# Kernel optimization log

Measured on AMD Instinct MI355X. Metric: run time of the kernel, lower is better.

## Reference

```python
import jax, jax.numpy as jnp
import numpy as np

D = 256   # input_dim (also per-head dim)
H = 8     # num_heads
B = 32
S = 1024


def setup_inputs() -> dict:
    key = jax.random.key(0)
    ks = jax.random.split(key, 9)
    scale = 1.0 / np.sqrt(D)
    x = jax.random.normal(ks[0], (B, S, D), dtype=jnp.float32)
    Wk = jax.random.normal(ks[1], (D, D * H), dtype=jnp.float32) * scale
    bk = jnp.zeros((D * H,), dtype=jnp.float32)
    Wv = jax.random.normal(ks[2], (D, D * H), dtype=jnp.float32) * scale
    bv = jnp.zeros((D * H,), dtype=jnp.float32)
    query = jax.random.normal(ks[3], (H, D), dtype=jnp.float32)
    Wo = jax.random.normal(ks[4], (D * H, D), dtype=jnp.float32) / np.sqrt(D * H)
    bo = jnp.zeros((D,), dtype=jnp.float32)
    return {"x": x, "Wk": Wk, "bk": bk, "Wv": Wv, "bv": bv,
            "query": query, "Wo": Wo, "bo": bo}


def reference(x, Wk, bk, Wv, bv, query, Wo, bo):
    b, s, _ = x.shape
    # keys/values: [B, S, H, D]
    keys = (x @ Wk + bk).reshape(b, s, H, D)
    values = (x @ Wv + bv).reshape(b, s, H, D)
    # per-head single-query scores over sequence: [B, S, H]
    scores = jnp.einsum("bshd,hd->bsh", keys, query)
    attn = jax.nn.softmax(scores, axis=1)
    # attention-pooled values per head: [B, H, D] -> concat [B, H*D]
    pooled = jnp.einsum("bsh,bshd->bhd", attn, values).reshape(b, H * D)
    return pooled @ Wo + bo
```

## Files before the change

### kernel.cpp

```cpp
#include <hip/hip_runtime.h>

#define D 256
#define H 8
#define B 32
#define S 1024
#define SCH 32
#define SCS 32
#define XPAD 4

#define OFF_QK   0
#define OFF_ML   2048
#define OFF_XWP  18432

__global__ void __launch_bounds__(256) k_prep(
        const float* __restrict__ Wk, const float* __restrict__ query,
        const float* __restrict__ bo, float* __restrict__ qk,
        float* __restrict__ out) {
    const int h  = blockIdx.x >> 5;
    const int kc = blockIdx.x & 31;
    const int t  = threadIdx.x;
    const int kl = t >> 5;
    const int dq = t & 31;
    const int k  = kc * 8 + kl;
    const int d0 = dq * 8;
    const float* wrow = Wk + (size_t)k * (D * H) + h * D + d0;
    const float* qrow = query + h * D + d0;
    const float4 w0 = *(const float4*)(wrow);
    const float4 w1 = *(const float4*)(wrow + 4);
    const float4 q0 = *(const float4*)(qrow);
    const float4 q1 = *(const float4*)(qrow + 4);
    float acc = w0.x * q0.x + w0.y * q0.y + w0.z * q0.z + w0.w * q0.w
              + w1.x * q1.x + w1.y * q1.y + w1.z * q1.z + w1.w * q1.w;
    #pragma unroll
    for (int msk = 1; msk < 32; msk <<= 1) acc += __shfl_xor(acc, msk);
    if (dq == 0) qk[h * D + k] = acc;
    if (h == 0) out[(size_t)kc * D + t] = bo[t];
}

__global__ void __launch_bounds__(256, 4) k_fused(
        const float* __restrict__ x, const float* __restrict__ qk,
        float* __restrict__ xwp, float2* __restrict__ mlbuf) {
    const int b  = blockIdx.x >> 5;
    const int c  = blockIdx.x & 31;
    const int s0 = c * SCS;
    const int t  = threadIdx.x;
    __shared__ float xL[SCS][D + XPAD];
    __shared__ float sc[SCS][H];
    {
        const int sl = t >> 3;
        const int dq = t & 7;
        const int d0 = dq * 32;
        const float* xrow = x + ((size_t)(b * S + s0 + sl)) * D + d0;
        float4 xr[8];
        #pragma unroll
        for (int j0 = 0; j0 < 8; j0++) {
            xr[j0] = *(const float4*)(xrow + j0 * 4);
            *(float4*)(&xL[sl][d0 + j0 * 4]) = xr[j0];
        }
        float accA[H];
        #pragma unroll
        for (int hh = 0; hh < H; hh++) {
            const float* qb = qk + hh * D + d0;
            float a = 0.f;
            #pragma unroll
            for (int j0 = 0; j0 < 8; j0++) {
                const float4 qv = *(const float4*)(qb + j0 * 4);
                a += xr[j0].x * qv.x + xr[j0].y * qv.y
                   + xr[j0].z * qv.z + xr[j0].w * qv.w;
            }
            accA[hh] = a;
        }
        #pragma unroll
        for (int hh = 0; hh < H; hh++) {
            accA[hh] += __shfl_xor(accA[hh], 1);
            accA[hh] += __shfl_xor(accA[hh], 2);
            accA[hh] += __shfl_xor(accA[hh], 4);
        }
        if (dq == 0) {
            #pragma unroll
            for (int hh = 0; hh < H; hh++) sc[sl][hh] = accA[hh];
        }
    }
    __syncthreads();

    {
        const int hh = t >> 5;
        const int u  = t & 31;
        const float v = sc[u][hh];
        float m = v;
        #pragma unroll
        for (int msk = 1; msk < 32; msk <<= 1) m = fmaxf(m, __shfl_xor(m, msk));
        const float e = __expf(v - m);
        float sum = e;
        #pragma unroll
        for (int msk = 1; msk < 32; msk <<= 1) sum += __shfl_xor(sum, msk);
        sc[u][hh] = e;
        if (u == 0) mlbuf[((size_t)(b * H + hh)) * SCH + c] = make_float2(m, sum);
    }
    __syncthreads();

    {
        float acc2[H] = {};
        #pragma unroll 8
        for (int s = 0; s < SCS; s++) {
            const float xv = xL[s][t];
            const float4 pa = *(const float4*)(&sc[s][0]);
            const float4 pb = *(const float4*)(&sc[s][4]);
            acc2[0] += pa.x * xv; acc2[1] += pa.y * xv;
            acc2[2] += pa.z * xv; acc2[3] += pa.w * xv;
            acc2[4] += pb.x * xv; acc2[5] += pb.y * xv;
            acc2[6] += pb.z * xv; acc2[7] += pb.w * xv;
        }
        #pragma unroll
        for (int hh = 0; hh < H; hh++)
            xwp[(((size_t)(b * H + hh)) * SCH + c) * D + t] = acc2[hh];
    }
}

__global__ void __launch_bounds__(256, 4) k_po(
        const float* __restrict__ xwp, const float2* __restrict__ mlbuf,
        const float* __restrict__ Wv, const float* __restrict__ bv,
        const float* __restrict__ Wo, float* __restrict__ out) {
    const int blk = blockIdx.x;
    const int dvq = blk & 3;
    const int bh  = blk >> 2;
    const int b = bh >> 3, h = bh & 7;
    const int t = threadIdx.x;
    __shared__ float scaleL[SCH];
    __shared__ float xwL[D];
    __shared__ float pp[256];
    __shared__ float pooledL[64];

    if (t < SCH) {
        const float2 ml = mlbuf[((size_t)(b * H + h)) * SCH + t];
        float M = ml.x;
        #pragma unroll
        for (int msk = 1; msk < 32; msk <<= 1) M = fmaxf(M, __shfl_xor(M, msk));
        const float p = __expf(ml.x - M);
        float L = ml.y * p;
        #pragma unroll
        for (int msk = 1; msk < 32; msk <<= 1) L += __shfl_xor(L, msk);
        scaleL[t] = p / L;
    }
    __syncthreads();
    {
        const float* xp = xwp + ((size_t)(b * H + h)) * SCH * D + t;
        float acc = 0.f;
        #pragma unroll 8
        for (int cc = 0; cc < SCH; cc++)
            acc += xp[(size_t)cc * D] * scaleL[cc];
        xwL[t] = acc;
    }
    __syncthreads();
    {
        const int kseg = t >> 6;
        const int dvl  = t & 63;
        const float* wp = Wv + (size_t)(kseg * 64) * (D * H) + h * D + dvq * 64 + dvl;
        float acc = 0.f;
        #pragma unroll 8
        for (int dd = 0; dd < 64; dd++)
            acc += xwL[kseg * 64 + dd] * wp[(size_t)dd * (D * H)];
        pp[t] = acc;
    }
    __syncthreads();
    if (t < 64)
        pooledL[t] = pp[t] + pp[t + 64] + pp[t + 128] + pp[t + 192]
                   + bv[h * D + dvq * 64 + t];
    __syncthreads();
    {
        const float* wo = Wo + (size_t)(h * D + dvq * 64) * D + t;
        float acc = 0.f;
        #pragma unroll 8
        for (int dv = 0; dv < 64; dv++)
            acc += pooledL[dv] * wo[(size_t)dv * D];
        atomicAdd(out + (size_t)b * D + t, acc);
    }
}

extern "C" void kernel_launch(void* const* d_in, const int* in_sizes, int n_in,
                              void* d_out, int out_size, void* d_ws, size_t ws_size,
                              hipStream_t stream) {
    const float* x     = (const float*)d_in[0];
    const float* Wk    = (const float*)d_in[1];
    const float* Wv    = (const float*)d_in[3];
    const float* bv    = (const float*)d_in[4];
    const float* query = (const float*)d_in[5];
    const float* Wo    = (const float*)d_in[6];
    const float* bo    = (const float*)d_in[7];
    float* out = (float*)d_out;
    float* ws  = (float*)d_ws;

    float*  qk    = ws + OFF_QK;
    float2* mlbuf = (float2*)(ws + OFF_ML);
    float*  xwp   = ws + OFF_XWP;

    k_prep<<<dim3(H * 32), dim3(256), 0, stream>>>(Wk, query, bo, qk, out);
    k_fused<<<dim3(B * SCH), dim3(256), 0, stream>>>(x, qk, xwp, mlbuf);
    k_po<<<dim3(B * H * 4), dim3(256), 0, stream>>>(xwp, mlbuf, Wv, bv, Wo, out);
}
```

Before: 129.6 us.

## Double sequence chunk per block, stage qk in LDS, keep x in registers

The fused score/pool kernel now runs 512-thread blocks over 64-position chunks, which halves the partial buffers that the reduction kernel reads. The qk vectors are staged in shared memory instead of being read from global per thread. The x tile is no longer copied into shared memory; each half of the block re-reads its 32 rows into registers for the weighted sum. The two halves' partials are combined through a shared-memory stage. Reading x twice from global and the higher register count may cost bandwidth and occupancy. A rotated load order is also added.

```diff
diff --git a/kernel.cpp b/kernel.cpp
--- a/kernel.cpp
+++ b/kernel.cpp
@@ -4,13 +4,12 @@
 #define H 8
 #define B 32
 #define S 1024
-#define SCH 32
-#define SCS 32
-#define XPAD 4
+#define SCH 16
+#define SCS 64
 
 #define OFF_QK   0
 #define OFF_ML   2048
-#define OFF_XWP  18432
+#define OFF_XWP  10240
 
 __global__ void __launch_bounds__(256) k_prep(
         const float* __restrict__ Wk, const float* __restrict__ query,
@@ -37,15 +36,18 @@
     if (h == 0) out[(size_t)kc * D + t] = bo[t];
 }
 
-__global__ void __launch_bounds__(256, 4) k_fused(
+__global__ void __launch_bounds__(512, 2) k_fused(
         const float* __restrict__ x, const float* __restrict__ qk,
         float* __restrict__ xwp, float2* __restrict__ mlbuf) {
-    const int b  = blockIdx.x >> 5;
-    const int c  = blockIdx.x & 31;
+    const int b  = blockIdx.x >> 4;
+    const int c  = blockIdx.x & 15;
     const int s0 = c * SCS;
     const int t  = threadIdx.x;
-    __shared__ float xL[SCS][D + XPAD];
+    __shared__ float qkL[H * D];
     __shared__ float sc[SCS][H];
+    ((float4*)qkL)[t] = ((const float4*)qk)[t];
+    __syncthreads();
+
     {
         const int sl = t >> 3;
         const int dq = t & 7;
@@ -54,17 +56,18 @@
         float4 xr[8];
         #pragma unroll
         for (int j0 = 0; j0 < 8; j0++) {
-            xr[j0] = *(const float4*)(xrow + j0 * 4);
-            *(float4*)(&xL[sl][d0 + j0 * 4]) = xr[j0];
+            const int je = (j0 + dq) & 7;
+            xr[j0] = *(const float4*)(xrow + je * 4);
         }
         float accA[H];
         #pragma unroll
         for (int hh = 0; hh < H; hh++) {
-            const float* qb = qk + hh * D + d0;
+            const float* qb = &qkL[hh * D + d0];
             float a = 0.f;
             #pragma unroll
             for (int j0 = 0; j0 < 8; j0++) {
-                const float4 qv = *(const float4*)(qb + j0 * 4);
+                const int je = (j0 + dq) & 7;
+                const float4 qv = *(const float4*)(qb + je * 4);
                 a += xr[j0].x * qv.x + xr[j0].y * qv.y
                    + xr[j0].z * qv.z + xr[j0].w * qv.w;
             }
@@ -81,39 +84,56 @@
             for (int hh = 0; hh < H; hh++) sc[sl][hh] = accA[hh];
         }
     }
-    __syncthreads();
-
-    {
-        const int hh = t >> 5;
-        const int u  = t & 31;
+
+    const int tt = t & 255;
+    const int sh = t >> 8;
+    float xv[32];
+    {
+        const float* xp = x + ((size_t)(b * S + s0 + sh * 32)) * D + tt;
+        #pragma unroll
+        for (int s = 0; s < 32; s++) xv[s] = xp[(size_t)s * D];
+    }
+    __syncthreads();
+
+    {
+        const int hh = t >> 6;
+        const int u  = t & 63;
         const float v = sc[u][hh];
         float m = v;
         #pragma unroll
-        for (int msk = 1; msk < 32; msk <<= 1) m = fmaxf(m, __shfl_xor(m, msk));
+        for (int msk = 1; msk < 64; msk <<= 1) m = fmaxf(m, __shfl_xor(m, msk));
         const float e = __expf(v - m);
         float sum = e;
         #pragma unroll
-        for (int msk = 1; msk < 32; msk <<= 1) sum += __shfl_xor(sum, msk);
+        for (int msk = 1; msk < 64; msk <<= 1) sum += __shfl_xor(sum, msk);
         sc[u][hh] = e;
         if (u == 0) mlbuf[((size_t)(b * H + hh)) * SCH + c] = make_float2(m, sum);
     }
     __syncthreads();
 
-    {
-        float acc2[H] = {};
-        #pragma unroll 8
-        for (int s = 0; s < SCS; s++) {
-            const float xv = xL[s][t];
-            const float4 pa = *(const float4*)(&sc[s][0]);
-            const float4 pb = *(const float4*)(&sc[s][4]);
-            acc2[0] += pa.x * xv; acc2[1] += pa.y * xv;
-            acc2[2] += pa.z * xv; acc2[3] += pa.w * xv;
-            acc2[4] += pb.x * xv; acc2[5] += pb.y * xv;
-            acc2[6] += pb.z * xv; acc2[7] += pb.w * xv;
-        }
-        #pragma unroll
-        for (int hh = 0; hh < H; hh++)
-            xwp[(((size_t)(b * H + hh)) * SCH + c) * D + t] = acc2[hh];
+    float acc2[H] = {};
+    #pragma unroll
+    for (int s = 0; s < 32; s++) {
+        const float4 pa = *(const float4*)(&sc[sh * 32 + s][0]);
+        const float4 pb = *(const float4*)(&sc[sh * 32 + s][4]);
+        acc2[0] += pa.x * xv[s]; acc2[1] += pa.y * xv[s];
+        acc2[2] += pa.z * xv[s]; acc2[3] += pa.w * xv[s];
+        acc2[4] += pb.x * xv[s]; acc2[5] += pb.y * xv[s];
+        acc2[6] += pb.z * xv[s]; acc2[7] += pb.w * xv[s];
+    }
+    {
+        float* stage = qkL;
+        if (sh == 1) {
+            #pragma unroll
+            for (int hh = 0; hh < H; hh++) stage[hh * 256 + tt] = acc2[hh];
+        }
+        __syncthreads();
+        if (sh == 0) {
+            #pragma unroll
+            for (int hh = 0; hh < H; hh++)
+                xwp[(((size_t)(b * H + hh)) * SCH + c) * D + tt]
+                    = acc2[hh] + stage[hh * 256 + tt];
+        }
     }
 }
 
@@ -135,18 +155,18 @@
         const float2 ml = mlbuf[((size_t)(b * H + h)) * SCH + t];
         float M = ml.x;
         #pragma unroll
-        for (int msk = 1; msk < 32; msk <<= 1) M = fmaxf(M, __shfl_xor(M, msk));
+        for (int msk = 1; msk < 16; msk <<= 1) M = fmaxf(M, __shfl_xor(M, msk));
         const float p = __expf(ml.x - M);
         float L = ml.y * p;
         #pragma unroll
-        for (int msk = 1; msk < 32; msk <<= 1) L += __shfl_xor(L, msk);
+        for (int msk = 1; msk < 16; msk <<= 1) L += __shfl_xor(L, msk);
         scaleL[t] = p / L;
     }
     __syncthreads();
     {
         const float* xp = xwp + ((size_t)(b * H + h)) * SCH * D + t;
         float acc = 0.f;
-        #pragma unroll 8
+        #pragma unroll
         for (int cc = 0; cc < SCH; cc++)
             acc += xp[(size_t)cc * D] * scaleL[cc];
         xwL[t] = acc;
@@ -195,6 +215,6 @@
     float*  xwp   = ws + OFF_XWP;
 
     k_prep<<<dim3(H * 32), dim3(256), 0, stream>>>(Wk, query, bo, qk, out);
-    k_fused<<<dim3(B * SCH), dim3(256), 0, stream>>>(x, qk, xwp, mlbuf);
+    k_fused<<<dim3(B * SCH), dim3(512), 0, stream>>>(x, qk, xwp, mlbuf);
     k_po<<<dim3(B * H * 4), dim3(256), 0, stream>>>(xwp, mlbuf, Wv, bv, Wo, out);
 }
```

Result: faster. 110.9 us (-14.4%).
